# Kernel tuning notes

Hardware: AMD Instinct MI355X
Metric: run time of the kernel (lower is better)

Reference implementation:

```python
import jax, jax.numpy as jnp
import numpy as np

X_SCALE, X_ZP = 0.03, -66.0
Y_SCALE, Y_ZP = 0.025, 160.0  # per-tensor quant params for uint8 y


def setup_inputs() -> dict:
    key = jax.random.key(0)
    kx, ky = jax.random.split(key)
    # x simulates int8 values in [-128, 127], stored as fp32
    x = jax.random.randint(kx, (7, 8, 1024, 1024), 0, 256).astype(jnp.float32) - 128.0
    # y simulates uint8 values in [0, 255], stored as fp32
    y = jax.random.randint(ky, (8, 1024, 1024), 0, 256).astype(jnp.float32)
    return {"x": x, "y": y}


def reference(x, y):
    # dequantize: (q - zero_point) * scale
    qx = (x - X_ZP) * X_SCALE              # [7, B, M, K] fp32
    qy = (y - Y_ZP) * Y_SCALE              # [B, K, N] fp32
    # torch.matmul broadcasting: 4D @ 3D -> [7, B, M, N]
    return jnp.einsum('sbmk,bkn->sbmn', qx, qy)
```

## Files before the change

kernel.cpp:

```cpp
#include <hip/hip_runtime.h>
#include <cstdint>


#define NG 56

typedef int v4i  __attribute__((ext_vector_type(4)));
typedef int v16i __attribute__((ext_vector_type(16)));

#define GLOAD16(g, l) __builtin_amdgcn_global_load_lds( \
    (const __attribute__((address_space(1))) void*)(g), \
    (__attribute__((address_space(3))) void*)(l), 16, 0, 0)

#define MFMA_I8(a, b, c) __builtin_amdgcn_mfma_i32_32x32x32_i8(a, b, c, 0, 0, 0)

typedef __attribute__((address_space(3))) const unsigned char* lds_cptr;

__device__ __forceinline__ v4i lds_read16(lds_cptr p) {
    v4i d;
    asm volatile("ds_read_b128 %0, %1" : "=v"(d) : "v"(p));
    return d;
}

__device__ __forceinline__ unsigned pack4(float4 v, float& s) {
    s += (v.x + v.y) + (v.z + v.w);
    unsigned b0 = __float_as_uint(v.x + 8388736.0f);
    unsigned b1 = __float_as_uint(v.y + 8388736.0f);
    unsigned b2 = __float_as_uint(v.z + 8388736.0f);
    unsigned b3 = __float_as_uint(v.w + 8388736.0f);
    return ((b0 & 0xFFu) | ((b1 & 0xFFu) << 8) | ((b2 & 0xFFu) << 16) | ((b3 & 0xFFu) << 24))
           ^ 0x80808080u;
}

__global__ __launch_bounds__(256) void k_prep_x(const float* __restrict__ x,
                                                unsigned char* __restrict__ xb,
                                                float* __restrict__ rx) {
    int row  = blockIdx.x * 4 + (threadIdx.x >> 6);
    int lane = threadIdx.x & 63;
    const float* src = x + (size_t)row * 1024;
    float s = 0.f;
#pragma unroll
    for (int it = 0; it < 4; ++it) {
        float4 v = *(const float4*)(src + it * 256 + lane * 4);
        unsigned p = pack4(v, s);
        *(unsigned*)&xb[(size_t)row * 1024 + it * 256 + lane * 4] = p;
    }
#pragma unroll
    for (int off = 32; off > 0; off >>= 1) s += __shfl_down(s, off);
    if (lane == 0) rx[row] = s;
}

__global__ __launch_bounds__(256) void k_prep_y(const float* __restrict__ y,
                                                unsigned char* __restrict__ yt,
                                                float* __restrict__ cy) {
    __shared__ float tile[64][65];
    __shared__ float csum[4][64];
    int b  = blockIdx.x >> 8;
    int t  = blockIdx.x & 255;
    int kt = (t >> 4) * 64, nt = (t & 15) * 64;
    int tx = threadIdx.x & 63;
    int ty = threadIdx.x >> 6;
    const float* src = y + ((size_t)b << 20) + (size_t)kt * 1024 + nt;
    float part = 0.f;
#pragma unroll
    for (int r = 0; r < 16; ++r) {
        int kk = r * 4 + ty;
        float v = src[(size_t)kk * 1024 + tx];
        tile[kk][tx] = v;
        part += v;
    }
    csum[ty][tx] = part;
    __syncthreads();
    if (threadIdx.x < 64) {
        float s = csum[0][tx] + csum[1][tx] + csum[2][tx] + csum[3][tx];
        atomicAdd(&cy[b * 1024 + nt + tx], s);
    }
    int ky = threadIdx.x & 15;
    int ny = threadIdx.x >> 4;
#pragma unroll
    for (int r = 0; r < 4; ++r) {
        int nn = r * 16 + ny;
        unsigned b0 = __float_as_uint(tile[ky * 4 + 0][nn] + 8388608.0f);
        unsigned b1 = __float_as_uint(tile[ky * 4 + 1][nn] + 8388608.0f);
        unsigned b2 = __float_as_uint(tile[ky * 4 + 2][nn] + 8388608.0f);
        unsigned b3 = __float_as_uint(tile[ky * 4 + 3][nn] + 8388608.0f);
        unsigned p = ((b0 & 0xFFu) | ((b1 & 0xFFu) << 8) | ((b2 & 0xFFu) << 16) |
                      ((b3 & 0xFFu) << 24)) ^ 0x80808080u;
        *(unsigned*)&yt[((size_t)b << 20) + (size_t)(nt + nn) * 1024 + kt + ky * 4] = p;
    }
}

__global__ __launch_bounds__(512, 2) void k_gemm(const unsigned char* __restrict__ xb,
                                                 const unsigned char* __restrict__ yt,
                                                 const float* __restrict__ rx,
                                                 const float* __restrict__ cy,
                                                 float* __restrict__ out) {
    __shared__ __align__(16) unsigned char As[4][256 * 64];

    int bid = blockIdx.x;
    int wg  = (bid & 7) * 112 + (bid >> 3);
    int g   = wg >> 4;
    int t   = wg & 15;
    int m0  = (t >> 2) * 256, n0 = (t & 3) * 256;
    int b   = g & 7;

    int tid = threadIdx.x, lane = tid & 63, w = tid >> 6;
    int wm = w >> 2, wn = w & 3;

    const unsigned char* Ab = xb + (size_t)g * 1048576 + (size_t)m0 * 1024;

    int srow   = tid >> 2;
    int schunk = (tid & 3) ^ ((srow >> 1) & 3);
    size_t offA0 = (size_t)srow * 1024 + (size_t)schunk * 16;
    size_t offA1 = offA0 + 131072;
    int dstA0 = (tid & ~63) * 16;
    int dstA1 = 8192 + (tid & ~63) * 16;

#define STAGE(buf, kbyte) do {                                    \
    GLOAD16(Ab + offA0 + (size_t)(kbyte), &As[buf][dstA0]);       \
    GLOAD16(Ab + offA1 + (size_t)(kbyte), &As[buf][dstA1]);       \
} while (0)

    v16i acc[4][2];
#pragma unroll
    for (int i = 0; i < 4; ++i)
#pragma unroll
        for (int j = 0; j < 2; ++j)
#pragma unroll
            for (int q = 0; q < 16; ++q) acc[i][j][q] = 0;

    int arow = lane & 31, hi = lane >> 5, key = (lane >> 1) & 3;
    int rA0 = (wm * 128 +  0 + arow) * 64;
    int rA1 = (wm * 128 + 32 + arow) * 64;
    int rA2 = (wm * 128 + 64 + arow) * 64;
    int rA3 = (wm * 128 + 96 + arow) * 64;
    int c0 = (hi ^ key) * 16;
    int c1 = ((2 + hi) ^ key) * 16;

    const unsigned char* Bbl = yt + ((size_t)b << 20)
                             + (size_t)(n0 + wn * 64 + arow) * 1024 + hi * 16;

#define LOADB(R0, R1, R2, R3, kbyte) do {                                             \
    const unsigned char* _bp = Bbl + (size_t)(kbyte);                                 \
    asm volatile("global_load_dwordx4 %0, %1, off" : "=&v"(R0) : "v"(_bp) : "memory");          \
    asm volatile("global_load_dwordx4 %0, %1, off" : "=&v"(R1) : "v"(_bp + 32) : "memory");     \
    asm volatile("global_load_dwordx4 %0, %1, off" : "=&v"(R2) : "v"(_bp + 32768) : "memory");  \
    asm volatile("global_load_dwordx4 %0, %1, off" : "=&v"(R3) : "v"(_bp + 32800) : "memory");  \
} while (0)

#define STEP(T, VMN, BU0, BU1, BU2, BU3, BL0, BL1, BL2, BL3, DOLB, DOST) do { \
    asm volatile("s_waitcnt vmcnt(" #VMN ")" ::: "memory");                   \
    __builtin_amdgcn_s_barrier();                                             \
    __builtin_amdgcn_sched_barrier(0);                                        \
    lds_cptr _ap = (lds_cptr)&As[(T) & 3][0];                                 \
    v4i a00 = lds_read16(_ap + rA0 + c0);                                     \
    v4i a10 = lds_read16(_ap + rA1 + c0);                                     \
    v4i a20 = lds_read16(_ap + rA2 + c0);                                     \
    v4i a30 = lds_read16(_ap + rA3 + c0);                                     \
    v4i a01 = lds_read16(_ap + rA0 + c1);                                     \
    v4i a11 = lds_read16(_ap + rA1 + c1);                                     \
    v4i a21 = lds_read16(_ap + rA2 + c1);                                     \
    v4i a31 = lds_read16(_ap + rA3 + c1);                                     \
    if (DOLB) { LOADB(BL0, BL1, BL2, BL3, ((T) + 1) * 64); }                  \
    __builtin_amdgcn_sched_barrier(0);                                        \
    if (DOST) { STAGE(((T) + 3) & 3, ((T) + 3) * 64); }                       \
    __builtin_amdgcn_sched_barrier(0);                                        \
    asm volatile("s_waitcnt lgkmcnt(0)" ::: "memory");                        \
    __builtin_amdgcn_sched_barrier(0);                                        \
    __builtin_amdgcn_s_setprio(1);                                            \
    acc[0][0] = MFMA_I8(a00, BU0, acc[0][0]);                                 \
    acc[1][0] = MFMA_I8(a10, BU0, acc[1][0]);                                 \
    acc[2][0] = MFMA_I8(a20, BU0, acc[2][0]);                                 \
    acc[3][0] = MFMA_I8(a30, BU0, acc[3][0]);                                 \
    acc[0][1] = MFMA_I8(a00, BU2, acc[0][1]);                                 \
    acc[1][1] = MFMA_I8(a10, BU2, acc[1][1]);                                 \
    acc[2][1] = MFMA_I8(a20, BU2, acc[2][1]);                                 \
    acc[3][1] = MFMA_I8(a30, BU2, acc[3][1]);                                 \
    acc[0][0] = MFMA_I8(a01, BU1, acc[0][0]);                                 \
    acc[1][0] = MFMA_I8(a11, BU1, acc[1][0]);                                 \
    acc[2][0] = MFMA_I8(a21, BU1, acc[2][0]);                                 \
    acc[3][0] = MFMA_I8(a31, BU1, acc[3][0]);                                 \
    acc[0][1] = MFMA_I8(a01, BU3, acc[0][1]);                                 \
    acc[1][1] = MFMA_I8(a11, BU3, acc[1][1]);                                 \
    acc[2][1] = MFMA_I8(a21, BU3, acc[2][1]);                                 \
    acc[3][1] = MFMA_I8(a31, BU3, acc[3][1]);                                 \
    __builtin_amdgcn_s_setprio(0);                                            \
} while (0)

    v4i bA0, bA1, bA2, bA3;
    v4i bB0, bB1, bB2, bB3;

    STAGE(0, 0);
    STAGE(1, 64);
    __builtin_amdgcn_sched_barrier(0);
    LOADB(bA0, bA1, bA2, bA3, 0);
    __builtin_amdgcn_sched_barrier(0);
    STAGE(2, 128);
    __builtin_amdgcn_sched_barrier(0);

#pragma unroll 1
    for (int T = 0; T < 14; T += 2) {
        STEP(T,     2, bA0, bA1, bA2, bA3, bB0, bB1, bB2, bB3, 1, (T < 13));
        STEP(T + 1, 2, bB0, bB1, bB2, bB3, bA0, bA1, bA2, bA3, 1, (T + 1 < 13));
    }
    STEP(14, 0, bA0, bA1, bA2, bA3, bB0, bB1, bB2, bB3, 1, 0);
    STEP(15, 0, bB0, bB1, bB2, bB3, bA0, bA1, bA2, bA3, 0, 0);
#undef STEP
#undef LOADB
#undef STAGE

    const float* rxp = rx + g * 1024 + m0 + wm * 128;
    const float* cyp = cy + b * 1024 + n0 + wn * 64;
    float* og = out + (size_t)g * 1048576 + (size_t)(m0 + wm * 128) * 1024 + n0 + wn * 64;
    int col = lane & 31, r4 = hi * 4;
#pragma unroll
    for (int fi = 0; fi < 4; ++fi)
#pragma unroll
        for (int fj = 0; fj < 2; ++fj) {
            int cc = fj * 32 + col;
            float cv = cyp[cc];
            v16i v = acc[fi][fj];
#pragma unroll
            for (int q = 0; q < 16; ++q) {
                int rl = (q & 3) + 8 * (q >> 2) + r4;
                float rxv = rxp[fi * 32 + rl];
                og[(size_t)(fi * 32 + rl) * 1024 + cc] =
                    7.5e-4f * ((float)v[q] - 32.0f * rxv + 66.0f * cv - 10813440.0f);
            }
        }
}

__global__ void k_naive(const float* __restrict__ x, const float* __restrict__ y,
                        float* __restrict__ out) {
    int g = blockIdx.z, b = g & 7;
    int tx = threadIdx.x, ty = threadIdx.y;
    int m = blockIdx.y * 16 + ty, n = blockIdx.x * 16 + tx;
    __shared__ float a[16][17], bs[16][17];
    float s = 0.f;
    for (int kt = 0; kt < 64; ++kt) {
        a[ty][tx]  = x[(size_t)g * 1048576 + (size_t)m * 1024 + kt * 16 + tx];
        bs[ty][tx] = y[(size_t)b * 1048576 + (size_t)(kt * 16 + ty) * 1024 + n];
        __syncthreads();
#pragma unroll
        for (int j = 0; j < 16; ++j)
            s += ((a[ty][j] + 66.0f) * 0.03f) * ((bs[j][tx] - 160.0f) * 0.025f);
        __syncthreads();
    }
    out[(size_t)g * 1048576 + (size_t)m * 1024 + n] = s;
}

extern "C" void kernel_launch(void* const* d_in, const int* in_sizes, int n_in,
                              void* d_out, int out_size, void* d_ws, size_t ws_size,
                              hipStream_t stream) {
    const float* x = (const float*)d_in[0];
    const float* y = (const float*)d_in[1];
    float* out = (float*)d_out;

    const size_t CY_OFF = 0;
    const size_t RX_OFF = 32768;
    const size_t YT_OFF = 262144;
    const size_t XB_OFF = 262144 + 8388608ull;
    const size_t NEED   = XB_OFF + 58720256ull;

    if (ws_size >= NEED) {
        float* cy         = (float*)((char*)d_ws + CY_OFF);
        float* rx         = (float*)((char*)d_ws + RX_OFF);
        unsigned char* yt = (unsigned char*)((char*)d_ws + YT_OFF);
        unsigned char* xb = (unsigned char*)((char*)d_ws + XB_OFF);
        hipMemsetAsync(cy, 0, 32768, stream);
        k_prep_x<<<14336, 256, 0, stream>>>(x, xb, rx);
        k_prep_y<<<2048, 256, 0, stream>>>(y, yt, cy);
        k_gemm<<<NG * 16, 512, 0, stream>>>(xb, yt, rx, cy, out);
    } else {
        dim3 grid(64, 64, NG), blk(16, 16);
        k_naive<<<grid, blk, 0, stream>>>(x, y, out);
    }
}
```

Measured before the change: 214.6 us.

## Fuse x int8 quantization and row sums into GEMM, stage B in LDS

```diff
diff --git a/kernel.cpp b/kernel.cpp
--- a/kernel.cpp
+++ b/kernel.cpp
@@ -4,8 +4,8 @@
 
 #define NG 56
 
-typedef int v4i  __attribute__((ext_vector_type(4)));
-typedef int v16i __attribute__((ext_vector_type(16)));
+typedef int   v4i  __attribute__((ext_vector_type(4)));
+typedef int   v16i __attribute__((ext_vector_type(16)));
 
 #define GLOAD16(g, l) __builtin_amdgcn_global_load_lds( \
     (const __attribute__((address_space(1))) void*)(g), \
@@ -21,32 +21,16 @@
     return d;
 }
 
-__device__ __forceinline__ unsigned pack4(float4 v, float& s) {
-    s += (v.x + v.y) + (v.z + v.w);
-    unsigned b0 = __float_as_uint(v.x + 8388736.0f);
-    unsigned b1 = __float_as_uint(v.y + 8388736.0f);
-    unsigned b2 = __float_as_uint(v.z + 8388736.0f);
-    unsigned b3 = __float_as_uint(v.w + 8388736.0f);
+__device__ __forceinline__ unsigned pk(v4i v, float& s) {
+    float x0 = __int_as_float(v[0]), x1 = __int_as_float(v[1]);
+    float x2 = __int_as_float(v[2]), x3 = __int_as_float(v[3]);
+    s += (x0 + x1) + (x2 + x3);
+    unsigned b0 = __float_as_uint(x0 + 8388736.0f);
+    unsigned b1 = __float_as_uint(x1 + 8388736.0f);
+    unsigned b2 = __float_as_uint(x2 + 8388736.0f);
+    unsigned b3 = __float_as_uint(x3 + 8388736.0f);
     return ((b0 & 0xFFu) | ((b1 & 0xFFu) << 8) | ((b2 & 0xFFu) << 16) | ((b3 & 0xFFu) << 24))
            ^ 0x80808080u;
-}
-
-__global__ __launch_bounds__(256) void k_prep_x(const float* __restrict__ x,
-                                                unsigned char* __restrict__ xb,
-                                                float* __restrict__ rx) {
-    int row  = blockIdx.x * 4 + (threadIdx.x >> 6);
-    int lane = threadIdx.x & 63;
-    const float* src = x + (size_t)row * 1024;
-    float s = 0.f;
-#pragma unroll
-    for (int it = 0; it < 4; ++it) {
-        float4 v = *(const float4*)(src + it * 256 + lane * 4);
-        unsigned p = pack4(v, s);
-        *(unsigned*)&xb[(size_t)row * 1024 + it * 256 + lane * 4] = p;
-    }
-#pragma unroll
-    for (int off = 32; off > 0; off >>= 1) s += __shfl_down(s, off);
-    if (lane == 0) rx[row] = s;
 }
 
 __global__ __launch_bounds__(256) void k_prep_y(const float* __restrict__ y,
@@ -89,12 +73,12 @@
     }
 }
 
-__global__ __launch_bounds__(512, 2) void k_gemm(const unsigned char* __restrict__ xb,
+__global__ __launch_bounds__(512, 2) void k_gemm(const float* __restrict__ xf,
                                                  const unsigned char* __restrict__ yt,
-                                                 const float* __restrict__ rx,
                                                  const float* __restrict__ cy,
                                                  float* __restrict__ out) {
-    __shared__ __align__(16) unsigned char As[4][256 * 64];
+    __shared__ __align__(16) unsigned char As[2][256 * 64];
+    __shared__ __align__(16) unsigned char Bs[3][256 * 64];
 
     int bid = blockIdx.x;
     int wg  = (bid & 7) * 112 + (bid >> 3);
@@ -106,109 +90,151 @@
     int tid = threadIdx.x, lane = tid & 63, w = tid >> 6;
     int wm = w >> 2, wn = w & 3;
 
-    const unsigned char* Ab = xb + (size_t)g * 1048576 + (size_t)m0 * 1024;
-
-    int srow   = tid >> 2;
-    int schunk = (tid & 3) ^ ((srow >> 1) & 3);
-    size_t offA0 = (size_t)srow * 1024 + (size_t)schunk * 16;
-    size_t offA1 = offA0 + 131072;
-    int dstA0 = (tid & ~63) * 16;
-    int dstA1 = 8192 + (tid & ~63) * 16;
-
-#define STAGE(buf, kbyte) do {                                    \
-    GLOAD16(Ab + offA0 + (size_t)(kbyte), &As[buf][dstA0]);       \
-    GLOAD16(Ab + offA1 + (size_t)(kbyte), &As[buf][dstA1]);       \
-} while (0)
-
-    v16i acc[4][2];
-#pragma unroll
-    for (int i = 0; i < 4; ++i)
-#pragma unroll
-        for (int j = 0; j < 2; ++j)
-#pragma unroll
-            for (int q = 0; q < 16; ++q) acc[i][j][q] = 0;
+    int r0   = tid >> 2;
+    int cg   = tid & 3;
+    int wkey = (tid >> 3) & 3;
+    int wadr0 = r0 * 64 + ((cg ^ wkey) * 16);
+    int wadr1 = wadr0 + 8192;
+    const float* Af0 = xf + (size_t)g * 1048576 + (size_t)(m0 + r0) * 1024 + cg * 16;
+    const float* Af1 = Af0 + 131072;
+
+    size_t soff0 = (size_t)r0 * 1024 + (size_t)((cg ^ wkey) * 16);
+    size_t soff1 = soff0 + 131072;
+    int bdst0 = (tid & ~63) * 16;
+    int bdst1 = 8192 + bdst0;
+    const unsigned char* Bb = yt + ((size_t)b << 20) + (size_t)n0 * 1024;
 
     int arow = lane & 31, hi = lane >> 5, key = (lane >> 1) & 3;
     int rA0 = (wm * 128 +  0 + arow) * 64;
     int rA1 = (wm * 128 + 32 + arow) * 64;
     int rA2 = (wm * 128 + 64 + arow) * 64;
     int rA3 = (wm * 128 + 96 + arow) * 64;
+    int rB0 = (wn * 64 +  0 + arow) * 64;
+    int rB1 = (wn * 64 + 32 + arow) * 64;
     int c0 = (hi ^ key) * 16;
     int c1 = ((2 + hi) ^ key) * 16;
 
-    const unsigned char* Bbl = yt + ((size_t)b << 20)
-                             + (size_t)(n0 + wn * 64 + arow) * 1024 + hi * 16;
-
-#define LOADB(R0, R1, R2, R3, kbyte) do {                                             \
-    const unsigned char* _bp = Bbl + (size_t)(kbyte);                                 \
-    asm volatile("global_load_dwordx4 %0, %1, off" : "=&v"(R0) : "v"(_bp) : "memory");          \
-    asm volatile("global_load_dwordx4 %0, %1, off" : "=&v"(R1) : "v"(_bp + 32) : "memory");     \
-    asm volatile("global_load_dwordx4 %0, %1, off" : "=&v"(R2) : "v"(_bp + 32768) : "memory");  \
-    asm volatile("global_load_dwordx4 %0, %1, off" : "=&v"(R3) : "v"(_bp + 32800) : "memory");  \
-} while (0)
-
-#define STEP(T, VMN, BU0, BU1, BU2, BU3, BL0, BL1, BL2, BL3, DOLB, DOST) do { \
-    asm volatile("s_waitcnt vmcnt(" #VMN ")" ::: "memory");                   \
-    __builtin_amdgcn_s_barrier();                                             \
-    __builtin_amdgcn_sched_barrier(0);                                        \
-    lds_cptr _ap = (lds_cptr)&As[(T) & 3][0];                                 \
-    v4i a00 = lds_read16(_ap + rA0 + c0);                                     \
-    v4i a10 = lds_read16(_ap + rA1 + c0);                                     \
-    v4i a20 = lds_read16(_ap + rA2 + c0);                                     \
-    v4i a30 = lds_read16(_ap + rA3 + c0);                                     \
-    v4i a01 = lds_read16(_ap + rA0 + c1);                                     \
-    v4i a11 = lds_read16(_ap + rA1 + c1);                                     \
-    v4i a21 = lds_read16(_ap + rA2 + c1);                                     \
-    v4i a31 = lds_read16(_ap + rA3 + c1);                                     \
-    if (DOLB) { LOADB(BL0, BL1, BL2, BL3, ((T) + 1) * 64); }                  \
-    __builtin_amdgcn_sched_barrier(0);                                        \
-    if (DOST) { STAGE(((T) + 3) & 3, ((T) + 3) * 64); }                       \
-    __builtin_amdgcn_sched_barrier(0);                                        \
-    asm volatile("s_waitcnt lgkmcnt(0)" ::: "memory");                        \
-    __builtin_amdgcn_sched_barrier(0);                                        \
-    __builtin_amdgcn_s_setprio(1);                                            \
-    acc[0][0] = MFMA_I8(a00, BU0, acc[0][0]);                                 \
-    acc[1][0] = MFMA_I8(a10, BU0, acc[1][0]);                                 \
-    acc[2][0] = MFMA_I8(a20, BU0, acc[2][0]);                                 \
-    acc[3][0] = MFMA_I8(a30, BU0, acc[3][0]);                                 \
-    acc[0][1] = MFMA_I8(a00, BU2, acc[0][1]);                                 \
-    acc[1][1] = MFMA_I8(a10, BU2, acc[1][1]);                                 \
-    acc[2][1] = MFMA_I8(a20, BU2, acc[2][1]);                                 \
-    acc[3][1] = MFMA_I8(a30, BU2, acc[3][1]);                                 \
-    acc[0][0] = MFMA_I8(a01, BU1, acc[0][0]);                                 \
-    acc[1][0] = MFMA_I8(a11, BU1, acc[1][0]);                                 \
-    acc[2][0] = MFMA_I8(a21, BU1, acc[2][0]);                                 \
-    acc[3][0] = MFMA_I8(a31, BU1, acc[3][0]);                                 \
-    acc[0][1] = MFMA_I8(a01, BU3, acc[0][1]);                                 \
-    acc[1][1] = MFMA_I8(a11, BU3, acc[1][1]);                                 \
-    acc[2][1] = MFMA_I8(a21, BU3, acc[2][1]);                                 \
-    acc[3][1] = MFMA_I8(a31, BU3, acc[3][1]);                                 \
-    __builtin_amdgcn_s_setprio(0);                                            \
-} while (0)
-
-    v4i bA0, bA1, bA2, bA3;
-    v4i bB0, bB1, bB2, bB3;
-
-    STAGE(0, 0);
-    STAGE(1, 64);
-    __builtin_amdgcn_sched_barrier(0);
-    LOADB(bA0, bA1, bA2, bA3, 0);
-    __builtin_amdgcn_sched_barrier(0);
-    STAGE(2, 128);
-    __builtin_amdgcn_sched_barrier(0);
+    v16i acc[4][2];
+#pragma unroll
+    for (int i = 0; i < 4; ++i)
+#pragma unroll
+        for (int j = 0; j < 2; ++j)
+#pragma unroll
+            for (int q = 0; q < 16; ++q) acc[i][j][q] = 0;
+
+    v4i fr0, fr1, fr2, fr3, fr4, fr5, fr6, fr7;
+    float rs0 = 0.f, rs1 = 0.f;
+
+#define LOADA(KT) do {                                                              \
+    const float* _p0 = Af0 + (KT) * 64;                                             \
+    const float* _p1 = Af1 + (KT) * 64;                                             \
+    asm volatile("global_load_dwordx4 %0, %1, off"           : "=&v"(fr0) : "v"(_p0) : "memory"); \
+    asm volatile("global_load_dwordx4 %0, %1, off offset:16" : "=&v"(fr1) : "v"(_p0) : "memory"); \
+    asm volatile("global_load_dwordx4 %0, %1, off offset:32" : "=&v"(fr2) : "v"(_p0) : "memory"); \
+    asm volatile("global_load_dwordx4 %0, %1, off offset:48" : "=&v"(fr3) : "v"(_p0) : "memory"); \
+    asm volatile("global_load_dwordx4 %0, %1, off"           : "=&v"(fr4) : "v"(_p1) : "memory"); \
+    asm volatile("global_load_dwordx4 %0, %1, off offset:16" : "=&v"(fr5) : "v"(_p1) : "memory"); \
+    asm volatile("global_load_dwordx4 %0, %1, off offset:32" : "=&v"(fr6) : "v"(_p1) : "memory"); \
+    asm volatile("global_load_dwordx4 %0, %1, off offset:48" : "=&v"(fr7) : "v"(_p1) : "memory"); \
+} while (0)
+
+#define PACKST(SLOT) do {                                                           \
+    unsigned q0 = pk(fr0, rs0), q1 = pk(fr1, rs0), q2 = pk(fr2, rs0), q3 = pk(fr3, rs0); \
+    v4i w0 = { (int)q0, (int)q1, (int)q2, (int)q3 };                                \
+    *(v4i*)&As[SLOT][wadr0] = w0;                                                   \
+    q0 = pk(fr4, rs1); q1 = pk(fr5, rs1); q2 = pk(fr6, rs1); q3 = pk(fr7, rs1);     \
+    v4i w1 = { (int)q0, (int)q1, (int)q2, (int)q3 };                                \
+    *(v4i*)&As[SLOT][wadr1] = w1;                                                   \
+} while (0)
+
+#define STAGEB(SLOT, KT) do {                                                       \
+    GLOAD16(Bb + soff0 + (size_t)(KT) * 64, &Bs[SLOT][bdst0]);                      \
+    GLOAD16(Bb + soff1 + (size_t)(KT) * 64, &Bs[SLOT][bdst1]);                      \
+} while (0)
+
+#define SB0 __builtin_amdgcn_sched_barrier(0)
+#define LGKM(N) asm volatile("s_waitcnt lgkmcnt(" #N ")" ::: "memory")
+
+#define MFMA4(I, A0_, A1_, B0_, B1_) do {                 \
+    __builtin_amdgcn_s_setprio(1);                        \
+    acc[I][0]     = MFMA_I8(A0_, B0_, acc[I][0]);         \
+    acc[I][1]     = MFMA_I8(A0_, B1_, acc[I][1]);         \
+    acc[I + 1][0] = MFMA_I8(A1_, B0_, acc[I + 1][0]);     \
+    acc[I + 1][1] = MFMA_I8(A1_, B1_, acc[I + 1][1]);     \
+    __builtin_amdgcn_s_setprio(0);                        \
+} while (0)
+
+#define VMW(N) asm volatile("s_waitcnt vmcnt(" #N ")" ::: "memory")
+
+#define TILE(SA, SBr, SBW, VMST, VMP3, DOB, DOA, DOP, KT) do {                      \
+    lds_cptr ap = (lds_cptr)&As[SA][0];                                             \
+    lds_cptr bp = (lds_cptr)&Bs[SBr][0];                                            \
+                                                                            \
+    VMST;                                                                           \
+    __builtin_amdgcn_s_barrier(); SB0;                                              \
+    v4i fa0 = lds_read16(ap + rA0 + c0);                                            \
+    v4i fa1 = lds_read16(ap + rA1 + c0);                                            \
+    v4i fb0 = lds_read16(bp + rB0 + c0);                                            \
+    v4i fb1 = lds_read16(bp + rB1 + c0);                                            \
+    v4i ga0 = lds_read16(ap + rA2 + c0);                                            \
+    v4i ga1 = lds_read16(ap + rA3 + c0);                                            \
+    LGKM(2); SB0;                                                                   \
+    MFMA4(0, fa0, fa1, fb0, fb1);                                                   \
+                                                                            \
+    __builtin_amdgcn_s_barrier(); SB0;                                              \
+    v4i ha0 = lds_read16(ap + rA0 + c1);                                            \
+    v4i ha1 = lds_read16(ap + rA1 + c1);                                            \
+    v4i hb0 = lds_read16(bp + rB0 + c1);                                            \
+    v4i hb1 = lds_read16(bp + rB1 + c1);                                            \
+    LGKM(4); SB0;                                                                   \
+    MFMA4(2, ga0, ga1, fb0, fb1);                                                   \
+                                                                            \
+    __builtin_amdgcn_s_barrier(); SB0;                                              \
+    v4i ia0 = lds_read16(ap + rA2 + c1);                                            \
+    v4i ia1 = lds_read16(ap + rA3 + c1);                                            \
+    if (DOB) { STAGEB(SBW, (KT) + 2); }                                             \
+    LGKM(2); SB0;                                                                   \
+    MFMA4(0, ha0, ha1, hb0, hb1);                                                   \
+                                                                            \
+    __builtin_amdgcn_s_barrier(); SB0;                                              \
+    VMP3; SB0;                                                                      \
+    if (DOP) { PACKST(((KT) + 1) & 1); }                                            \
+    if (DOA) { LOADA((KT) + 2); }                                                   \
+    LGKM(0); SB0;                                                                   \
+    MFMA4(2, ia0, ia1, hb0, hb1);                                                   \
+} while (0)
+
+    LOADA(0); SB0;
+    STAGEB(0, 0);
+    STAGEB(1, 1); SB0;
+    VMW(4); SB0;
+    PACKST(0);
+    LOADA(1); SB0;
+    LGKM(0); SB0;
 
 #pragma unroll 1
-    for (int T = 0; T < 14; T += 2) {
-        STEP(T,     2, bA0, bA1, bA2, bA3, bB0, bB1, bB2, bB3, 1, (T < 13));
-        STEP(T + 1, 2, bB0, bB1, bB2, bB3, bA0, bA1, bA2, bA3, 1, (T + 1 < 13));
-    }
-    STEP(14, 0, bA0, bA1, bA2, bA3, bB0, bB1, bB2, bB3, 1, 0);
-    STEP(15, 0, bB0, bB1, bB2, bB3, bA0, bA1, bA2, bA3, 0, 0);
-#undef STEP
-#undef LOADB
-#undef STAGE
-
-    const float* rxp = rx + g * 1024 + m0 + wm * 128;
+    for (int rr = 0; rr < 2; ++rr) {
+        int KT = rr * 6;
+        TILE(0, 0, 2, VMW(10), VMW(2), 1, 1, 1, (KT + 0));
+        TILE(1, 1, 0, VMW(10), VMW(2), 1, 1, 1, (KT + 1));
+        TILE(0, 2, 1, VMW(10), VMW(2), 1, 1, 1, (KT + 2));
+        TILE(1, 0, 2, VMW(10), VMW(2), 1, 1, 1, (KT + 3));
+        TILE(0, 1, 0, VMW(10), VMW(2), 1, 1, 1, (KT + 4));
+        TILE(1, 2, 1, VMW(10), VMW(2), 1, 1, 1, (KT + 5));
+    }
+    TILE(0, 0, 2, VMW(10), VMW(2), 1, 1, 1, 12);
+    TILE(1, 1, 0, VMW(10), VMW(2), 1, 1, 1, 13);
+    TILE(0, 2, 0, VMW(10), VMW(0), 0, 0, 1, 14);
+    TILE(1, 0, 0, VMW(0),  (void)0, 0, 0, 0, 15);
+#undef TILE
+
+    rs0 += __shfl_xor(rs0, 1); rs0 += __shfl_xor(rs0, 2);
+    rs1 += __shfl_xor(rs1, 1); rs1 += __shfl_xor(rs1, 2);
+    float* rxs = (float*)&As[0][0];
+    __syncthreads();
+    if ((tid & 3) == 0) { rxs[r0] = rs0; rxs[r0 + 128] = rs1; }
+    __syncthreads();
+
     const float* cyp = cy + b * 1024 + n0 + wn * 64;
     float* og = out + (size_t)g * 1048576 + (size_t)(m0 + wm * 128) * 1024 + n0 + wn * 64;
     int col = lane & 31, r4 = hi * 4;
@@ -222,11 +248,18 @@
 #pragma unroll
             for (int q = 0; q < 16; ++q) {
                 int rl = (q & 3) + 8 * (q >> 2) + r4;
-                float rxv = rxp[fi * 32 + rl];
+                float rxv = rxs[wm * 128 + fi * 32 + rl];
                 og[(size_t)(fi * 32 + rl) * 1024 + cc] =
                     7.5e-4f * ((float)v[q] - 32.0f * rxv + 66.0f * cv - 10813440.0f);
             }
         }
+#undef LOADA
+#undef PACKST
+#undef STAGEB
+#undef MFMA4
+#undef LGKM
+#undef VMW
+#undef SB0
 }
 
 __global__ void k_naive(const float* __restrict__ x, const float* __restrict__ y,
@@ -256,20 +289,15 @@
     float* out = (float*)d_out;
 
     const size_t CY_OFF = 0;
-    const size_t RX_OFF = 32768;
     const size_t YT_OFF = 262144;
-    const size_t XB_OFF = 262144 + 8388608ull;
-    const size_t NEED   = XB_OFF + 58720256ull;
+    const size_t NEED   = YT_OFF + 8388608ull;
 
     if (ws_size >= NEED) {
         float* cy         = (float*)((char*)d_ws + CY_OFF);
-        float* rx         = (float*)((char*)d_ws + RX_OFF);
         unsigned char* yt = (unsigned char*)((char*)d_ws + YT_OFF);
-        unsigned char* xb = (unsigned char*)((char*)d_ws + XB_OFF);
         hipMemsetAsync(cy, 0, 32768, stream);
-        k_prep_x<<<14336, 256, 0, stream>>>(x, xb, rx);
         k_prep_y<<<2048, 256, 0, stream>>>(y, yt, cy);
-        k_gemm<<<NG * 16, 512, 0, stream>>>(xb, yt, rx, cy, out);
+        k_gemm<<<NG * 16, 512, 0, stream>>>(x, yt, cy, out);
     } else {
         dim3 grid(64, 64, NG), blk(16, 16);
         k_naive<<<grid, blk, 0, stream>>>(x, y, out);
```

New measurement: 663.8 us. +209.3%, slower.
